# Kernel optimization log

Measured on AMD Instinct MI355X. Metric: run time of the kernel, lower is better.

Reference implementation:

```python
import jax, jax.numpy as jnp
import numpy as np

B, S, D = 4, 2048, 1024
H = 16
DH = D // H


def setup_inputs() -> dict:
    key = jax.random.key(0)
    ks = jax.random.split(key, 5)
    scale = 0.02
    return {
        "x": jax.random.normal(ks[0], (B, S, D), dtype=jnp.float32),
        "w_in": jax.random.normal(ks[1], (D, 3 * D), dtype=jnp.float32) * scale,
        "b_in": jax.random.normal(ks[2], (3 * D,), dtype=jnp.float32) * scale,
        "w_out": jax.random.normal(ks[3], (D, D), dtype=jnp.float32) * scale,
        "b_out": jax.random.normal(ks[4], (D,), dtype=jnp.float32) * scale,
        "causal_mask": 1,
    }


def reference(x, w_in, b_in, w_out, b_out, causal_mask):
    b, s, d = x.shape
    qkv = x @ w_in + b_in                       # [B,S,3D]
    q, k, v = jnp.split(qkv, 3, axis=-1)
    # [B,S,D] -> [B,H,S,DH]
    q = q.reshape(b, s, H, DH).transpose(0, 2, 1, 3)
    k = k.reshape(b, s, H, DH).transpose(0, 2, 1, 3)
    v = v.reshape(b, s, H, DH).transpose(0, 2, 1, 3)
    scores = jnp.einsum("bhqd,bhkd->bhqk", q, k)
    if causal_mask:
        # mask applied before scaling in original; -inf unaffected by scaling
        mask = jnp.triu(jnp.ones((s, s), dtype=bool), k=1)
        scores = jnp.where(mask, -jnp.inf, scores)
    scores = scores / jnp.sqrt(jnp.float32(DH))
    probs = jax.nn.softmax(scores, axis=-1)
    out = jnp.einsum("bhqk,bhkd->bhqd", probs, v)
    out = out.transpose(0, 2, 1, 3).reshape(b, s, d)
    return out @ w_out + b_out
```

## Files before the change

### kernel.cpp

```cpp
#include <hip/hip_runtime.h>
#include <hip/hip_bf16.h>
#include <cstdint>

#define NB 4
#define NS 2048
#define ND 1024
#define NH 16
#define NDH 64
#define NM (NB*NS)
#define N3D (3*ND)

typedef __attribute__((ext_vector_type(8))) short short8;
typedef __attribute__((ext_vector_type(4))) float f32x4;
typedef __attribute__((ext_vector_type(4))) unsigned short us4;
typedef __attribute__((ext_vector_type(4))) unsigned int uint4v;

__device__ __forceinline__ float bf2f(unsigned short u) {
  unsigned int i = ((unsigned int)u) << 16;
  return __builtin_bit_cast(float, i);
}
__device__ __forceinline__ unsigned short f2bf(float f) {
  unsigned int i = __builtin_bit_cast(unsigned int, f);
  i = (i + 0x7FFFu + ((i >> 16) & 1u)) >> 16;
  return (unsigned short)i;
}
__device__ __forceinline__ unsigned int cvtpk_bf16(float lo, float hi) {
  unsigned int r;
  asm("v_cvt_pk_bf16_f32 %0, %1, %2" : "=v"(r) : "v"(lo), "v"(hi));
  return r;
}

#define GLD16(g, l) __builtin_amdgcn_global_load_lds( \
    (__attribute__((address_space(1))) void*)(void*)(g), \
    (__attribute__((address_space(3))) void*)(l), 16, 0, 0)

__global__ __launch_bounds__(256) void cvt_bf16_k(
    const float* __restrict__ in, unsigned short* __restrict__ out, int n)
{
  const int i = (blockIdx.x * 256 + threadIdx.x) * 4;
  if (i + 3 < n) {
    const f32x4 v = *(const f32x4*)(in + i);
    us4 o = {f2bf(v[0]), f2bf(v[1]), f2bf(v[2]), f2bf(v[3])};
    *(us4*)(out + i) = o;
  }
}

__global__ __launch_bounds__(256) void transpose_cvt_k(
    const float* __restrict__ in, unsigned short* __restrict__ out,
    int rows, int cols)
{
  __shared__ unsigned short tile[32][33];
  const int c0 = blockIdx.x * 32, r0 = blockIdx.y * 32;
  const int tx = threadIdx.x & 31, ty = threadIdx.x >> 5;
  #pragma unroll
  for (int i = ty; i < 32; i += 8)
    tile[i][tx] = f2bf(in[(size_t)(r0 + i) * cols + (c0 + tx)]);
  __syncthreads();
  #pragma unroll
  for (int i = ty; i < 32; i += 8)
    out[(size_t)(c0 + i) * rows + (r0 + tx)] = tile[tx][i];
}

__global__ __launch_bounds__(256) void vt_transpose_k(
    const unsigned short* __restrict__ qkv, unsigned short* __restrict__ vt)
{
  __shared__ unsigned short tile[32][33];
  const int dt = blockIdx.x & 1;
  const int st = (blockIdx.x >> 1) & 63;
  const int bh = blockIdx.x >> 7;
  const int b = bh >> 4, h = bh & 15;
  const int tx = threadIdx.x & 31, ty = threadIdx.x >> 5;
  const int s0 = st * 32, d0 = dt * 32;
  const unsigned short* src = qkv + (size_t)b * NS * N3D + 2 * ND + h * NDH;
  #pragma unroll
  for (int i = ty; i < 32; i += 8)
    tile[i][tx] = src[(size_t)(s0 + i) * N3D + d0 + tx];
  __syncthreads();
  unsigned short* dst = vt + (size_t)bh * NDH * NS;
  #pragma unroll
  for (int i = ty; i < 32; i += 8)
    dst[(size_t)(d0 + i) * NS + s0 + tx] = tile[tx][i];
}

template<bool OUT_F32>
__global__ __launch_bounds__(256) void gemm_bt_bias(
    const unsigned short* __restrict__ A,
    const unsigned short* __restrict__ Bt,
    const float* __restrict__ bias,
    unsigned short* __restrict__ Cb,
    float* __restrict__ Cf,
    int M, int N, int K)
{
  __shared__ __align__(16) unsigned short Alds[128 * 32];
  __shared__ __align__(16) unsigned short Blds[128 * 32];
  const int nbn = N >> 7;
  const int nwg = (M >> 7) * nbn;
  const int cpx = nwg >> 3;
  const int tid = (blockIdx.x & 7) * cpx + (blockIdx.x >> 3);
  const int bm = tid / nbn, bn = tid % nbn;
  const int m0 = bm << 7, n0 = bn << 7;
  const int w = threadIdx.x >> 6, l = threadIdx.x & 63;
  const int wr = w >> 1, wc = w & 1;
  const int lr = l & 15, lg = l >> 4;

  const unsigned short* gA = A + (size_t)(m0 + w * 32 + (l >> 2)) * K + (l & 3) * 8;
  const unsigned short* gB = Bt + (size_t)(n0 + w * 32 + (l >> 2)) * K + (l & 3) * 8;
  unsigned short* lA = Alds + (w * 32) * 32;
  unsigned short* lB = Blds + (w * 32) * 32;

  f32x4 acc[4][4] = {};

  for (int k0 = 0; k0 < K; k0 += 32) {
    GLD16(gA + k0, lA);
    GLD16(gA + k0 + (size_t)16 * K, lA + 16 * 32);
    GLD16(gB + k0, lB);
    GLD16(gB + k0 + (size_t)16 * K, lB + 16 * 32);
    __syncthreads();

    short8 a[4], b[4];
    #pragma unroll
    for (int i = 0; i < 4; ++i)
      a[i] = *(const short8*)(Alds + (wr * 64 + i * 16 + lr) * 32 + lg * 8);
    #pragma unroll
    for (int j = 0; j < 4; ++j)
      b[j] = *(const short8*)(Blds + (wc * 64 + j * 16 + lr) * 32 + lg * 8);

    #pragma unroll
    for (int i = 0; i < 4; ++i)
      #pragma unroll
      for (int j = 0; j < 4; ++j)
        acc[i][j] = __builtin_amdgcn_mfma_f32_16x16x32_bf16(a[i], b[j], acc[i][j], 0, 0, 0);
    __syncthreads();
  }

  #pragma unroll
  for (int j = 0; j < 4; ++j) {
    const int col = n0 + wc * 64 + j * 16 + lr;
    const float bv = bias[col];
    #pragma unroll
    for (int i = 0; i < 4; ++i) {
      #pragma unroll
      for (int r = 0; r < 4; ++r) {
        const int row = m0 + wr * 64 + i * 16 + lg * 4 + r;
        const float v = acc[i][j][r] + bv;
        if (OUT_F32) Cf[(size_t)row * N + col] = v;
        else         Cb[(size_t)row * N + col] = f2bf(v);
      }
    }
  }
}

__global__ __launch_bounds__(512) void attn_fwd(
    const unsigned short* __restrict__ qkv,
    const unsigned short* __restrict__ Vt,
    unsigned short* __restrict__ out)
{
  __shared__ __align__(16) char Kl[2][64 * 128];
  __shared__ __align__(16) char Vl[2][64 * 128];

  const int bid = blockIdx.x;
  const int bh = bid & 63;
  const int slot = bid >> 6;
  const int b = bh >> 4, h = bh & 15;
  const int w = threadIdx.x >> 6, l = threadIdx.x & 63;
  const int lr = l & 15, lg = l >> 4;

  const size_t rs = N3D;
  const unsigned short* Qb = qkv + (size_t)b * NS * rs + (size_t)h * NDH;
  const unsigned short* Kb = Qb + ND;
  const unsigned short* VtB = Vt + (size_t)bh * NDH * NS;

  const int srow = l >> 3;
  const int sw = (((l & 7) * 16) ^ (srow << 4)) >> 1;
  const unsigned short* KsrcBase = Kb + (size_t)(8 * w + srow) * rs + sw;
  const unsigned short* VsrcBase = VtB + (size_t)(8 * w + srow) * NS + sw;
  const int ldsRow0 = (8 * w) * 128;

  const float QSCALE = 0.125f * 1.44269504f;
  const int ksw = (lr & 7) << 4;

  #pragma unroll 1
  for (int pass = 0; pass < 2; ++pass) {
    const int qt = pass == 0 ? slot : 15 - slot;
    const int q0 = qt * 128 + w * 16;
    const int T = 2 * qt + 2;

    short8 qf[2];
    {
      const unsigned short* qrow = Qb + (size_t)(q0 + lr) * rs + lg * 8;
      qf[0] = *(const short8*)(qrow);
      qf[1] = *(const short8*)(qrow + 32);
      #pragma unroll
      for (int j = 0; j < 8; ++j) {
        qf[0][j] = (short)f2bf(bf2f((unsigned short)qf[0][j]) * QSCALE);
        qf[1][j] = (short)f2bf(bf2f((unsigned short)qf[1][j]) * QSCALE);
      }
    }

    float l_run = 0.f;
    f32x4 o[4] = {};

    auto stage = [&](int buf, int kt) {
      const int kb = kt << 6;
      GLD16(KsrcBase + (size_t)kb * rs, &Kl[buf][ldsRow0]);
      GLD16(VsrcBase + kb,              &Vl[buf][ldsRow0]);
    };

    stage(0, 0);
    __syncthreads();

    #pragma unroll 1
    for (int kt = 0; kt < T; ++kt) {
      const int cur = kt & 1;
      if (kt + 1 < T) stage(cur ^ 1, kt + 1);
      const int kbase = kt << 6;

      if (kbase <= q0 + 15) {
        short8 kf[4][2];
        #pragma unroll
        for (int ks = 0; ks < 4; ++ks) {
          const char* rowp = &Kl[cur][(ks * 16 + lr) * 128];
          kf[ks][0] = *(const short8*)(rowp + ((lg * 16) ^ ksw));
          kf[ks][1] = *(const short8*)(rowp + ((64 + lg * 16) ^ ksw));
        }

        f32x4 s[4] = {};
        #pragma unroll
        for (int ks = 0; ks < 4; ++ks) {
          s[ks] = __builtin_amdgcn_mfma_f32_16x16x32_bf16(kf[ks][0], qf[0], s[ks], 0, 0, 0);
          s[ks] = __builtin_amdgcn_mfma_f32_16x16x32_bf16(kf[ks][1], qf[1], s[ks], 0, 0, 0);
        }

        short8 vf[4][2];
        #pragma unroll
        for (int nb = 0; nb < 4; ++nb) {
          const char* rowp = &Vl[cur][(nb * 16 + lr) * 128];
          vf[nb][0] = *(const short8*)(rowp + ((lg * 16) ^ ksw));
          vf[nb][1] = *(const short8*)(rowp + ((64 + lg * 16) ^ ksw));
        }

        const bool domask = (kbase + 63 > q0);
        const int qi = q0 + lr;
        float p[16];
        if (domask) {
          #pragma unroll
          for (int ks = 0; ks < 4; ++ks)
            #pragma unroll
            for (int r = 0; r < 4; ++r)
              p[ks * 4 + r] = (kbase + ks * 16 + lg * 4 + r > qi)
                                ? 0.f : exp2f(s[ks][r]);
        } else {
          #pragma unroll
          for (int ks = 0; ks < 4; ++ks)
            #pragma unroll
            for (int r = 0; r < 4; ++r)
              p[ks * 4 + r] = exp2f(s[ks][r]);
        }
        float s0 = (p[0] + p[1]) + (p[2] + p[3]);
        float s1 = (p[4] + p[5]) + (p[6] + p[7]);
        float s2 = (p[8] + p[9]) + (p[10] + p[11]);
        float s3 = (p[12] + p[13]) + (p[14] + p[15]);
        l_run += (s0 + s1) + (s2 + s3);

        unsigned A0 = cvtpk_bf16(p[0],  p[1]),  B0 = cvtpk_bf16(p[2],  p[3]);
        unsigned A1 = cvtpk_bf16(p[4],  p[5]),  B1 = cvtpk_bf16(p[6],  p[7]);
        unsigned A2 = cvtpk_bf16(p[8],  p[9]),  B2 = cvtpk_bf16(p[10], p[11]);
        unsigned A3 = cvtpk_bf16(p[12], p[13]), B3 = cvtpk_bf16(p[14], p[15]);

        asm("v_permlane32_swap_b32 %0, %1" : "+v"(A0), "+v"(A1));
        asm("v_permlane16_swap_b32 %0, %1" : "+v"(A0), "+v"(A1));
        asm("v_permlane32_swap_b32 %0, %1" : "+v"(B0), "+v"(B1));
        asm("v_permlane16_swap_b32 %0, %1" : "+v"(B0), "+v"(B1));
        asm("v_permlane32_swap_b32 %0, %1" : "+v"(A2), "+v"(A3));
        asm("v_permlane16_swap_b32 %0, %1" : "+v"(A2), "+v"(A3));
        asm("v_permlane32_swap_b32 %0, %1" : "+v"(B2), "+v"(B3));
        asm("v_permlane16_swap_b32 %0, %1" : "+v"(B2), "+v"(B3));

        uint4v u0 = {A0, B0, A1, B1};
        uint4v u1 = {A2, B2, A3, B3};
        short8 pf0 = __builtin_bit_cast(short8, u0);
        short8 pf1 = __builtin_bit_cast(short8, u1);

        #pragma unroll
        for (int nb = 0; nb < 4; ++nb)
          o[nb] = __builtin_amdgcn_mfma_f32_16x16x32_bf16(pf0, vf[nb][0], o[nb], 0, 0, 0);
        #pragma unroll
        for (int nb = 0; nb < 4; ++nb)
          o[nb] = __builtin_amdgcn_mfma_f32_16x16x32_bf16(pf1, vf[nb][1], o[nb], 0, 0, 0);
      }

      __syncthreads();
    }

    {
      float lt = l_run;
      lt += __shfl_xor(lt, 16);
      lt += __shfl_xor(lt, 32);
      #pragma unroll
      for (int rr = 0; rr < 4; ++rr) {
        const float lq = __shfl(lt, lg * 4 + rr);
        const float inv = 1.0f / lq;
        const int qi = q0 + lg * 4 + rr;
        #pragma unroll
        for (int nb = 0; nb < 4; ++nb)
          out[(size_t)(b * NS + qi) * ND + h * NDH + nb * 16 + lr] = f2bf(o[nb][rr] * inv);
      }
    }
  }
}

extern "C" void kernel_launch(void* const* d_in, const int* in_sizes, int n_in,
                              void* d_out, int out_size, void* d_ws, size_t ws_size,
                              hipStream_t stream) {
  const float* x     = (const float*)d_in[0];
  const float* w_in  = (const float*)d_in[1];
  const float* b_in  = (const float*)d_in[2];
  const float* w_out = (const float*)d_in[3];
  const float* b_out = (const float*)d_in[4];
  float* out = (float*)d_out;

  char* ws = (char*)d_ws;
  size_t off = 0;
  unsigned short* x_bf    = (unsigned short*)(ws + off); off += (size_t)NM * ND * 2;
  unsigned short* qkv     = (unsigned short*)(ws + off); off += (size_t)NM * N3D * 2;
  unsigned short* attn    = (unsigned short*)(ws + off); off += (size_t)NM * ND * 2;
  unsigned short* w_in_t  = (unsigned short*)(ws + off); off += (size_t)N3D * ND * 2;
  unsigned short* w_out_t = (unsigned short*)(ws + off); off += (size_t)ND * ND * 2;
  unsigned short* vt = x_bf;

  cvt_bf16_k<<<dim3((NM * ND) / (256 * 4)), 256, 0, stream>>>(x, x_bf, NM * ND);
  transpose_cvt_k<<<dim3(N3D / 32, ND / 32), 256, 0, stream>>>(w_in, w_in_t, ND, N3D);
  transpose_cvt_k<<<dim3(ND / 32, ND / 32), 256, 0, stream>>>(w_out, w_out_t, ND, ND);

  gemm_bt_bias<false><<<dim3((NM / 128) * (N3D / 128)), 256, 0, stream>>>(
      x_bf, w_in_t, b_in, qkv, nullptr, NM, N3D, ND);

  vt_transpose_k<<<dim3(64 * 64 * 2), 256, 0, stream>>>(qkv, vt);

  attn_fwd<<<dim3(64 * 8), 512, 0, stream>>>(qkv, vt, attn);

  gemm_bt_bias<true><<<dim3((NM / 128) * (ND / 128)), 256, 0, stream>>>(
      attn, w_out_t, b_out, nullptr, out, NM, ND, ND);
}
```

Before: 203.2 us.

## Double-buffer GEMM LDS tiles and XOR-swizzle layout to avoid bank conflicts

After: 192.0 us. 1.06x faster.

```diff
diff --git a/kernel.cpp b/kernel.cpp
--- a/kernel.cpp
+++ b/kernel.cpp
@@ -91,8 +91,8 @@
     float* __restrict__ Cf,
     int M, int N, int K)
 {
-  __shared__ __align__(16) unsigned short Alds[128 * 32];
-  __shared__ __align__(16) unsigned short Blds[128 * 32];
+  __shared__ __align__(16) unsigned short Alds[2][128 * 32];
+  __shared__ __align__(16) unsigned short Blds[2][128 * 32];
   const int nbn = N >> 7;
   const int nwg = (M >> 7) * nbn;
   const int cpx = nwg >> 3;
@@ -103,33 +103,46 @@
   const int wr = w >> 1, wc = w & 1;
   const int lr = l & 15, lg = l >> 4;
 
-  const unsigned short* gA = A + (size_t)(m0 + w * 32 + (l >> 2)) * K + (l & 3) * 8;
-  const unsigned short* gB = Bt + (size_t)(n0 + w * 32 + (l >> 2)) * K + (l & 3) * 8;
-  unsigned short* lA = Alds + (w * 32) * 32;
-  unsigned short* lB = Blds + (w * 32) * 32;
+  const int sc = (l & 3) ^ ((l >> 2) & 3);
+  const unsigned short* gA = A + (size_t)(m0 + w * 32 + (l >> 2)) * K + sc * 8;
+  const unsigned short* gB = Bt + (size_t)(n0 + w * 32 + (l >> 2)) * K + sc * 8;
+  const int lwoff = (w * 32) * 32;
+
+  auto stage = [&](int buf, int k0) {
+    unsigned short* la = &Alds[buf][lwoff];
+    unsigned short* lb = &Blds[buf][lwoff];
+    GLD16(gA + k0, la);
+    GLD16(gA + k0 + (size_t)16 * K, la + 16 * 32);
+    GLD16(gB + k0, lb);
+    GLD16(gB + k0 + (size_t)16 * K, lb + 16 * 32);
+  };
 
   f32x4 acc[4][4] = {};
-
-  for (int k0 = 0; k0 < K; k0 += 32) {
-    GLD16(gA + k0, lA);
-    GLD16(gA + k0 + (size_t)16 * K, lA + 16 * 32);
-    GLD16(gB + k0, lB);
-    GLD16(gB + k0 + (size_t)16 * K, lB + 16 * 32);
-    __syncthreads();
+  const int rc = lr & 3;
+
+  stage(0, 0);
+  __syncthreads();
+
+  #pragma unroll 2
+  for (int it = 0; it < (K >> 5); ++it) {
+    const int buf = it & 1;
+    const int k0 = it << 5;
+    if (k0 + 32 < K) stage(buf ^ 1, k0 + 32);
 
     short8 a[4], b[4];
     #pragma unroll
     for (int i = 0; i < 4; ++i)
-      a[i] = *(const short8*)(Alds + (wr * 64 + i * 16 + lr) * 32 + lg * 8);
+      a[i] = *(const short8*)(&Alds[buf][(wr * 64 + i * 16 + lr) * 32 + ((lg ^ rc) << 3)]);
     #pragma unroll
     for (int j = 0; j < 4; ++j)
-      b[j] = *(const short8*)(Blds + (wc * 64 + j * 16 + lr) * 32 + lg * 8);
+      b[j] = *(const short8*)(&Blds[buf][(wc * 64 + j * 16 + lr) * 32 + ((lg ^ rc) << 3)]);
 
     #pragma unroll
     for (int i = 0; i < 4; ++i)
       #pragma unroll
       for (int j = 0; j < 4; ++j)
         acc[i][j] = __builtin_amdgcn_mfma_f32_16x16x32_bf16(a[i], b[j], acc[i][j], 0, 0, 0);
+
     __syncthreads();
   }
 
```
